# Kernel optimization log

Measured on AMD Instinct MI355X. Metric: run time of the kernel, lower is better.

## Reference

```python
import jax, jax.numpy as jnp
import numpy as np

B, N, D = 8, 2048, 1024


def setup_inputs() -> dict:
    key = jax.random.key(0)
    k1, k2, k3, k4 = jax.random.split(key, 4)
    x = jax.random.normal(k1, (B, N, D), dtype=jnp.float32)
    f = jax.random.normal(k2, (B, N, D), dtype=jnp.float32)
    # nn.Linear(D, 1, bias=False) weights, shape [1, D]
    lim = 1.0 / np.sqrt(D)
    wk = jax.random.uniform(k3, (1, D), dtype=jnp.float32, minval=-lim, maxval=lim)
    wq = jax.random.uniform(k4, (1, D), dtype=jnp.float32, minval=-lim, maxval=lim)
    return {"x": x, "f": f, "wk": wk, "wq": wq}


def reference(x, f, wk, wq):
    # scalar k/q projections: [B, N]
    k = jnp.einsum("bnd,d->bn", x, wk[0])
    q = jnp.einsum("bnd,d->bn", x, wq[0])
    scale = 1.0 / jnp.sqrt(jnp.float32(D))
    # rank-1 outer-product scores: e[b,i,j] = k[b,i]*q[b,j]/sqrt(D)
    e = k[:, :, None] * q[:, None, :] * scale  # [B, N, N]
    # keep upper triangle (incl. diag), then any exact zero -> -inf
    # (faithful to torch: e_post[e_post == 0] = -inf, which also hits
    #  naturally-zero upper-triangle entries)
    e_tri = jnp.triu(e)
    e_post = jnp.where(e_tri == 0, -jnp.inf, e_tri)
    a = jax.nn.softmax(e_post, axis=1)  # softmax over rows (dim=1)
    # f_out = a^T @ f
    f_out = jnp.einsum("bij,bid->bjd", a, f)
    return f_out
```

## Files before the change

kernel.cpp:

```cpp
#include <hip/hip_runtime.h>

#define B 8
#define N 2048
#define D 1024
#define C 32
#define LC (N / C)
#define M 6

__global__ __launch_bounds__(256) void k_proj(const float* __restrict__ x,
                                              const float* __restrict__ wk,
                                              const float* __restrict__ wq,
                                              float* __restrict__ kq) {
    const int wave = threadIdx.x >> 6;
    const int lane = threadIdx.x & 63;
    const int row  = blockIdx.x * 4 + wave;
    const float4* xr  = (const float4*)(x + (size_t)row * D);
    const float4* wk4 = (const float4*)wk;
    const float4* wq4 = (const float4*)wq;
    float ak = 0.f, aq = 0.f;
#pragma unroll
    for (int t = 0; t < (D / 4) / 64; ++t) {
        float4 xv = xr[t * 64 + lane];
        float4 kv = wk4[t * 64 + lane];
        float4 qv = wq4[t * 64 + lane];
        ak += xv.x * kv.x + xv.y * kv.y + xv.z * kv.z + xv.w * kv.w;
        aq += xv.x * qv.x + xv.y * qv.y + xv.z * qv.z + xv.w * qv.w;
    }
#pragma unroll
    for (int off = 32; off > 0; off >>= 1) {
        ak += __shfl_down(ak, off, 64);
        aq += __shfl_down(aq, off, 64);
    }
    if (lane == 0) {
        kq[row] = ak;
        kq[B * N + row] = aq;
    }
}

__global__ __launch_bounds__(64) void k_scanT(const float* __restrict__ kq,
                                              float* __restrict__ Tc) {
    __shared__ float lds[C][M];
    const int b = blockIdx.x;
    const int c = threadIdx.x;
    if (c < C) {
        float tm[M] = {0.f, 0.f, 0.f, 0.f, 0.f, 0.f};
        const float* kb = kq + b * N + c * LC;
        for (int i = 0; i < LC; ++i) {
            float kk = kb[i];
            tm[0] += (kk != 0.0f) ? 1.0f : 0.0f;
            float kp = kk;
#pragma unroll
            for (int m = 1; m < M; ++m) { tm[m] += kp; kp *= kk; }
        }
#pragma unroll
        for (int m = 0; m < M; ++m) lds[c][m] = tm[m];
    }
    __syncthreads();
    if (threadIdx.x == 0) {
        float run[M] = {0.f, 0.f, 0.f, 0.f, 0.f, 0.f};
        for (int c2 = 0; c2 < C; ++c2) {
#pragma unroll
            for (int m = 0; m < M; ++m) {
                Tc[(b * C + c2) * M + m] = run[m];
                run[m] += lds[c2][m];
            }
        }
    }
}

__global__ __launch_bounds__(256) void k_partial(const float* __restrict__ kq,
                                                 const float* __restrict__ f,
                                                 float* __restrict__ part) {
    const int bi   = blockIdx.x;
    const int dblk = bi & 3;
    const int c    = (bi >> 2) & (C - 1);
    const int b    = bi >> 7;
    const int d    = dblk * 256 + threadIdx.x;
    const float* kb = kq + b * N + c * LC;
    const float* fb = f + (size_t)(b * N + c * LC) * D + d;
    float s[M] = {0.f, 0.f, 0.f, 0.f, 0.f, 0.f};
    for (int i = 0; i < LC; ++i) {
        float kk = kb[i];
        float ff = fb[(size_t)i * D];
        s[0] += (kk != 0.0f) ? ff : 0.0f;
        float kp = kk;
#pragma unroll
        for (int m = 1; m < M; ++m) { s[m] += kp * ff; kp *= kk; }
    }
    const size_t base = (size_t)(b * C + c) * M * D + d;
#pragma unroll
    for (int m = 0; m < M; ++m) part[base + (size_t)m * D] = s[m];
}

__global__ __launch_bounds__(256) void k_scanP(float* __restrict__ part) {
    const int gid = blockIdx.x * 256 + threadIdx.x;
    const int d   = gid & (D - 1);
    const int m   = (gid >> 10) % M;
    const int b   = gid / (D * M);
    float run = 0.f;
    for (int c = 0; c < C; ++c) {
        const size_t idx = (size_t)(b * C + c) * M * D + (size_t)m * D + d;
        float v = part[idx];
        part[idx] = run;
        run += v;
    }
}

__global__ __launch_bounds__(256) void k_out(const float* __restrict__ kq,
                                             const float* __restrict__ f,
                                             const float* __restrict__ Tc,
                                             const float* __restrict__ part,
                                             float* __restrict__ out) {
    const int bi   = blockIdx.x;
    const int dblk = bi & 3;
    const int c    = (bi >> 2) & (C - 1);
    const int b    = bi >> 7;
    const int d    = dblk * 256 + threadIdx.x;

    float s[M], t[M];
    const size_t pbase = (size_t)(b * C + c) * M * D + d;
#pragma unroll
    for (int m = 0; m < M; ++m) s[m] = part[pbase + (size_t)m * D];
#pragma unroll
    for (int m = 0; m < M; ++m) t[m] = Tc[(b * C + c) * M + m];

    const float* kb = kq + b * N + c * LC;
    const float* qb = kq + B * N + b * N + c * LC;
    const float* fb = f + (size_t)(b * N + c * LC) * D + d;
    float*       ob = out + (size_t)(b * N + c * LC) * D + d;

    for (int i = 0; i < LC; ++i) {
        float kk = kb[i];
        float qq = qb[i];
        float ff = fb[(size_t)i * D];
        float w = (kk != 0.0f) ? 1.0f : 0.0f;
        t[0] += w;
        s[0] += w * ff;
        float kp = kk;
#pragma unroll
        for (int m = 1; m < M; ++m) { t[m] += kp; s[m] += kp * ff; kp *= kk; }

        const float cj = qq * 0.03125f;
        const float g1 = cj;
        const float g2 = 0.5f * cj * g1;
        const float g3 = (1.0f / 3.0f) * cj * g2;
        const float g4 = 0.25f * cj * g3;
        const float g5 = 0.2f * cj * g4;
        float Z   = t[0] + g1 * t[1] + g2 * t[2] + g3 * t[3] + g4 * t[4] + g5 * t[5];
        float num = s[0] + g1 * s[1] + g2 * s[2] + g3 * s[3] + g4 * s[4] + g5 * s[5];
        ob[(size_t)i * D] = num * __builtin_amdgcn_rcpf(Z);
    }
}

extern "C" void kernel_launch(void* const* d_in, const int* in_sizes, int n_in,
                              void* d_out, int out_size, void* d_ws, size_t ws_size,
                              hipStream_t stream) {
    (void)in_sizes; (void)n_in; (void)out_size; (void)ws_size;
    const float* x  = (const float*)d_in[0];
    const float* f  = (const float*)d_in[1];
    const float* wk = (const float*)d_in[2];
    const float* wq = (const float*)d_in[3];
    float* out = (float*)d_out;
    float* ws  = (float*)d_ws;

    float* kq   = ws;
    float* Tc   = ws + 2 * B * N;
    float* part = ws + 2 * B * N + 4096;

    hipLaunchKernelGGL(k_proj,    dim3(B * N / 4),        dim3(256), 0, stream, x, wk, wq, kq);
    hipLaunchKernelGGL(k_scanT,   dim3(B),                dim3(64),  0, stream, kq, Tc);
    hipLaunchKernelGGL(k_partial, dim3(B * C * (D/256)),  dim3(256), 0, stream, kq, f, part);
    hipLaunchKernelGGL(k_scanP,   dim3(B * M * D / 256),  dim3(256), 0, stream, part);
    hipLaunchKernelGGL(k_out,     dim3(B * C * (D/256)),  dim3(256), 0, stream, kq, f, Tc, part, out);
}
```

Before: 201.1 us.

## Vectorize partial/out kernels with float4, double chunk count, merge scan kernels

Switches the chunk-partial and output kernels to float4 loads and stores, with 128-thread blocks each covering half of D. The chunk count goes from 32 to 64, which shortens each serial chunk loop and raises the block count. The two scan kernels are merged into one launch, with the partial scan also vectorized, and the polynomial evaluation is rewritten in Horner form. The aim is fewer memory instructions, more parallelism and one less launch, at the cost of a larger partial buffer and more registers per thread.

After: 202.0 us. Within noise of the previous version (+0.5%).

```diff
diff --git a/kernel.cpp b/kernel.cpp
--- a/kernel.cpp
+++ b/kernel.cpp
@@ -3,7 +3,7 @@
 #define B 8
 #define N 2048
 #define D 1024
-#define C 32
+#define C 64
 #define LC (N / C)
 #define M 6
 
@@ -37,118 +37,136 @@
     }
 }
 
-__global__ __launch_bounds__(64) void k_scanT(const float* __restrict__ kq,
-                                              float* __restrict__ Tc) {
-    __shared__ float lds[C][M];
-    const int b = blockIdx.x;
-    const int c = threadIdx.x;
-    if (c < C) {
-        float tm[M] = {0.f, 0.f, 0.f, 0.f, 0.f, 0.f};
-        const float* kb = kq + b * N + c * LC;
-        for (int i = 0; i < LC; ++i) {
-            float kk = kb[i];
-            tm[0] += (kk != 0.0f) ? 1.0f : 0.0f;
-            float kp = kk;
+__global__ __launch_bounds__(128) void k_partial(const float* __restrict__ kq,
+                                                 const float* __restrict__ f,
+                                                 float* __restrict__ part) {
+    const int dhalf = blockIdx.x & 1;
+    const int c     = (blockIdx.x >> 1) & (C - 1);
+    const int b     = blockIdx.x >> 7;
+    const int d     = dhalf * 512 + threadIdx.x * 4;
+    const float*  kb = kq + b * N + c * LC;
+    const float4* fb = (const float4*)(f + (size_t)(b * N + c * LC) * D + d);
+    float4 s[M];
 #pragma unroll
-            for (int m = 1; m < M; ++m) { tm[m] += kp; kp *= kk; }
+    for (int m = 0; m < M; ++m) s[m] = make_float4(0.f, 0.f, 0.f, 0.f);
+#pragma unroll 8
+    for (int i = 0; i < LC; ++i) {
+        float4 ff = fb[i * (D / 4)];
+        float  kk = kb[i];
+        float  w  = (kk != 0.0f) ? 1.0f : 0.0f;
+        s[0].x += w * ff.x; s[0].y += w * ff.y; s[0].z += w * ff.z; s[0].w += w * ff.w;
+        float kp = kk;
+#pragma unroll
+        for (int m = 1; m < M; ++m) {
+            s[m].x += kp * ff.x; s[m].y += kp * ff.y;
+            s[m].z += kp * ff.z; s[m].w += kp * ff.w;
+            kp *= kk;
         }
+    }
+    float4* pb = (float4*)(part + ((size_t)(b * C + c) * M) * D + d);
 #pragma unroll
-        for (int m = 0; m < M; ++m) lds[c][m] = tm[m];
-    }
-    __syncthreads();
-    if (threadIdx.x == 0) {
-        float run[M] = {0.f, 0.f, 0.f, 0.f, 0.f, 0.f};
-        for (int c2 = 0; c2 < C; ++c2) {
+    for (int m = 0; m < M; ++m) pb[m * (D / 4)] = s[m];
+}
+
+__global__ __launch_bounds__(256) void k_scan(const float* __restrict__ kq,
+                                              float* __restrict__ Tc,
+                                              float* __restrict__ part) {
+    if (blockIdx.x < B) {
+        __shared__ float lds[C][M];
+        const int b = blockIdx.x;
+        const int c = threadIdx.x;
+        if (c < C) {
+            float tm[M] = {0.f, 0.f, 0.f, 0.f, 0.f, 0.f};
+            const float* kb = kq + b * N + c * LC;
 #pragma unroll
-            for (int m = 0; m < M; ++m) {
-                Tc[(b * C + c2) * M + m] = run[m];
-                run[m] += lds[c2][m];
+            for (int i = 0; i < LC; ++i) {
+                float kk = kb[i];
+                tm[0] += (kk != 0.0f) ? 1.0f : 0.0f;
+                float kp = kk;
+#pragma unroll
+                for (int m = 1; m < M; ++m) { tm[m] += kp; kp *= kk; }
             }
+#pragma unroll
+            for (int m = 0; m < M; ++m) lds[c][m] = tm[m];
+        }
+        __syncthreads();
+        if (threadIdx.x == 0) {
+            float run[M] = {0.f, 0.f, 0.f, 0.f, 0.f, 0.f};
+            for (int c2 = 0; c2 < C; ++c2) {
+#pragma unroll
+                for (int m = 0; m < M; ++m) {
+                    Tc[(b * C + c2) * M + m] = run[m];
+                    run[m] += lds[c2][m];
+                }
+            }
+        }
+    } else {
+        const int gid = (blockIdx.x - B) * 256 + threadIdx.x;
+        const int d   = (gid & (D / 4 - 1)) * 4;
+        const int m   = (gid >> 8) % M;
+        const int b   = gid / (256 * M);
+        float4 run = make_float4(0.f, 0.f, 0.f, 0.f);
+        for (int c = 0; c < C; ++c) {
+            float4* p = (float4*)(part + ((size_t)(b * C + c) * M + m) * D + d);
+            float4 v = *p;
+            *p = run;
+            run.x += v.x; run.y += v.y; run.z += v.z; run.w += v.w;
         }
     }
 }
 
-__global__ __launch_bounds__(256) void k_partial(const float* __restrict__ kq,
-                                                 const float* __restrict__ f,
-                                                 float* __restrict__ part) {
-    const int bi   = blockIdx.x;
-    const int dblk = bi & 3;
-    const int c    = (bi >> 2) & (C - 1);
-    const int b    = bi >> 7;
-    const int d    = dblk * 256 + threadIdx.x;
-    const float* kb = kq + b * N + c * LC;
-    const float* fb = f + (size_t)(b * N + c * LC) * D + d;
-    float s[M] = {0.f, 0.f, 0.f, 0.f, 0.f, 0.f};
-    for (int i = 0; i < LC; ++i) {
-        float kk = kb[i];
-        float ff = fb[(size_t)i * D];
-        s[0] += (kk != 0.0f) ? ff : 0.0f;
-        float kp = kk;
-#pragma unroll
-        for (int m = 1; m < M; ++m) { s[m] += kp * ff; kp *= kk; }
-    }
-    const size_t base = (size_t)(b * C + c) * M * D + d;
-#pragma unroll
-    for (int m = 0; m < M; ++m) part[base + (size_t)m * D] = s[m];
-}
-
-__global__ __launch_bounds__(256) void k_scanP(float* __restrict__ part) {
-    const int gid = blockIdx.x * 256 + threadIdx.x;
-    const int d   = gid & (D - 1);
-    const int m   = (gid >> 10) % M;
-    const int b   = gid / (D * M);
-    float run = 0.f;
-    for (int c = 0; c < C; ++c) {
-        const size_t idx = (size_t)(b * C + c) * M * D + (size_t)m * D + d;
-        float v = part[idx];
-        part[idx] = run;
-        run += v;
-    }
-}
-
-__global__ __launch_bounds__(256) void k_out(const float* __restrict__ kq,
+__global__ __launch_bounds__(128) void k_out(const float* __restrict__ kq,
                                              const float* __restrict__ f,
                                              const float* __restrict__ Tc,
                                              const float* __restrict__ part,
                                              float* __restrict__ out) {
-    const int bi   = blockIdx.x;
-    const int dblk = bi & 3;
-    const int c    = (bi >> 2) & (C - 1);
-    const int b    = bi >> 7;
-    const int d    = dblk * 256 + threadIdx.x;
+    const int dhalf = blockIdx.x & 1;
+    const int c     = (blockIdx.x >> 1) & (C - 1);
+    const int b     = blockIdx.x >> 7;
+    const int d     = dhalf * 512 + threadIdx.x * 4;
 
-    float s[M], t[M];
-    const size_t pbase = (size_t)(b * C + c) * M * D + d;
+    float4 s[M];
+    float  t[M];
+    const float4* pb = (const float4*)(part + ((size_t)(b * C + c) * M) * D + d);
 #pragma unroll
-    for (int m = 0; m < M; ++m) s[m] = part[pbase + (size_t)m * D];
+    for (int m = 0; m < M; ++m) s[m] = pb[m * (D / 4)];
 #pragma unroll
     for (int m = 0; m < M; ++m) t[m] = Tc[(b * C + c) * M + m];
 
-    const float* kb = kq + b * N + c * LC;
-    const float* qb = kq + B * N + b * N + c * LC;
-    const float* fb = f + (size_t)(b * N + c * LC) * D + d;
-    float*       ob = out + (size_t)(b * N + c * LC) * D + d;
+    const float*  kb = kq + b * N + c * LC;
+    const float*  qb = kq + B * N + b * N + c * LC;
+    const float4* fb = (const float4*)(f + (size_t)(b * N + c * LC) * D + d);
+    float4*       ob = (float4*)(out + (size_t)(b * N + c * LC) * D + d);
 
+#pragma unroll 4
     for (int i = 0; i < LC; ++i) {
-        float kk = kb[i];
-        float qq = qb[i];
-        float ff = fb[(size_t)i * D];
-        float w = (kk != 0.0f) ? 1.0f : 0.0f;
+        float4 ff = fb[i * (D / 4)];
+        float  kk = kb[i];
+        float  qq = qb[i];
+        float  w  = (kk != 0.0f) ? 1.0f : 0.0f;
         t[0] += w;
-        s[0] += w * ff;
+        s[0].x += w * ff.x; s[0].y += w * ff.y; s[0].z += w * ff.z; s[0].w += w * ff.w;
         float kp = kk;
 #pragma unroll
-        for (int m = 1; m < M; ++m) { t[m] += kp; s[m] += kp * ff; kp *= kk; }
-
+        for (int m = 1; m < M; ++m) {
+            t[m] += kp;
+            s[m].x += kp * ff.x; s[m].y += kp * ff.y;
+            s[m].z += kp * ff.z; s[m].w += kp * ff.w;
+            kp *= kk;
+        }
         const float cj = qq * 0.03125f;
-        const float g1 = cj;
-        const float g2 = 0.5f * cj * g1;
-        const float g3 = (1.0f / 3.0f) * cj * g2;
-        const float g4 = 0.25f * cj * g3;
-        const float g5 = 0.2f * cj * g4;
-        float Z   = t[0] + g1 * t[1] + g2 * t[2] + g3 * t[3] + g4 * t[4] + g5 * t[5];
-        float num = s[0] + g1 * s[1] + g2 * s[2] + g3 * s[3] + g4 * s[4] + g5 * s[5];
-        ob[(size_t)i * D] = num * __builtin_amdgcn_rcpf(Z);
+        const float g2 = cj * 0.5f;
+        const float g3 = cj * (1.0f / 3.0f);
+        const float g4 = cj * 0.25f;
+        const float g5 = cj * 0.2f;
+        float Z = ((((t[5] * g5 + t[4]) * g4 + t[3]) * g3 + t[2]) * g2 + t[1]) * cj + t[0];
+        float rz = __builtin_amdgcn_rcpf(Z);
+        float4 o;
+        o.x = (((((s[5].x * g5 + s[4].x) * g4 + s[3].x) * g3 + s[2].x) * g2 + s[1].x) * cj + s[0].x) * rz;
+        o.y = (((((s[5].y * g5 + s[4].y) * g4 + s[3].y) * g3 + s[2].y) * g2 + s[1].y) * cj + s[0].y) * rz;
+        o.z = (((((s[5].z * g5 + s[4].z) * g4 + s[3].z) * g3 + s[2].z) * g2 + s[1].z) * cj + s[0].z) * rz;
+        o.w = (((((s[5].w * g5 + s[4].w) * g4 + s[3].w) * g3 + s[2].w) * g2 + s[1].w) * cj + s[0].w) * rz;
+        ob[i * (D / 4)] = o;
     }
 }
 
@@ -167,9 +185,8 @@
     float* Tc   = ws + 2 * B * N;
     float* part = ws + 2 * B * N + 4096;
 
-    hipLaunchKernelGGL(k_proj,    dim3(B * N / 4),        dim3(256), 0, stream, x, wk, wq, kq);
-    hipLaunchKernelGGL(k_scanT,   dim3(B),                dim3(64),  0, stream, kq, Tc);
-    hipLaunchKernelGGL(k_partial, dim3(B * C * (D/256)),  dim3(256), 0, stream, kq, f, part);
-    hipLaunchKernelGGL(k_scanP,   dim3(B * M * D / 256),  dim3(256), 0, stream, part);
-    hipLaunchKernelGGL(k_out,     dim3(B * C * (D/256)),  dim3(256), 0, stream, kq, f, Tc, part, out);
+    hipLaunchKernelGGL(k_proj,    dim3(B * N / 4),          dim3(256), 0, stream, x, wk, wq, kq);
+    hipLaunchKernelGGL(k_partial, dim3(B * C * 2),          dim3(128), 0, stream, kq, f, part);
+    hipLaunchKernelGGL(k_scan,    dim3(B + B * M * D / 1024), dim3(256), 0, stream, kq, Tc, part);
+    hipLaunchKernelGGL(k_out,     dim3(B * C * 2),          dim3(128), 0, stream, kq, f, Tc, part, out);
 }
```
